# Performance work log

Hardware: AMD Instinct MI355X
Metric: run time of the kernel (lower is better)

Reference implementation:

```python
import jax, jax.numpy as jnp
import numpy as np

USER_NUM = 100000
ITEM_NUM = 100000  # padding index; table has ITEM_NUM+1 rows
D = 64
B = 4096
L = 200
NEG_WEIGHT = 0.1


def setup_inputs() -> dict:
    key = jax.random.key(0)
    k1, k2, k3, k4, k5 = jax.random.split(key, 5)
    uids = jax.random.randint(k1, (B,), 0, USER_NUM, dtype=jnp.int64 if jax.config.jax_enable_x64 else jnp.int32)
    pos_iids = jax.random.randint(k2, (B, L), 0, ITEM_NUM + 1, dtype=jnp.int64 if jax.config.jax_enable_x64 else jnp.int32)
    user_W = jax.random.normal(k3, (USER_NUM, D), dtype=jnp.float32) * 0.1
    item_W = jax.random.normal(k4, (ITEM_NUM + 1, D), dtype=jnp.float32) * 0.1
    h = jnp.full((D, 1), 0.01, dtype=jnp.float32)  # reset_para: constant 0.01
    return {"uids": uids, "pos_iids": pos_iids, "user_W": user_W, "item_W": item_W, "h": h}


def reference(uids, pos_iids, user_W, item_W, h):
    u_emb = user_W[uids]                      # [B, D] (dropout p=0 -> identity)
    pos_embs = item_W[pos_iids]               # [B, L, D]
    mask = (pos_iids != ITEM_NUM).astype(u_emb.dtype)  # padding id masked out
    pos_embs = pos_embs * mask[:, :, None]
    # hpq[b,l] = sum_d u[b,d] * pos[b,l,d] * h[d]
    hpq = jnp.einsum('bd,bld,d->bl', u_emb, pos_embs, h[:, 0])
    pos_data_loss = jnp.sum((1.0 - NEG_WEIGHT) * jnp.square(hpq) - 2.0 * hpq)
    # part_1/part_2 in torch are sums of per-row outer products == Gram matrices
    part_1 = item_W.T @ item_W                # [D, D]
    part_2 = u_emb.T @ u_emb                  # [D, D]
    part_3 = h @ h.T                          # [D, D]
    all_data_loss = jnp.sum(part_1 * part_2 * part_3)
    return NEG_WEIGHT * all_data_loss + pos_data_loss
```

## Files before the change

### kernel.cpp

```cpp
#include <hip/hip_runtime.h>

#define D 64
#define ITEM_PAD 100000
#define LSEQ 200
#define BATCH 4096
#define NEG_W 0.1f
#define NBI 512
#define NBU 64


__global__ void gram_kernel(const float* __restrict__ W, const int* __restrict__ idx,
                            int nrows, float* __restrict__ out, int partial) {
    __shared__ float tile[16 * D];
    const int t  = threadIdx.x;
    const int ti = t >> 4;
    const int tj = t & 15;

    float acc[4][4] = {{0.f,0.f,0.f,0.f},{0.f,0.f,0.f,0.f},
                       {0.f,0.f,0.f,0.f},{0.f,0.f,0.f,0.f}};

    const int nchunks = (nrows + 15) >> 4;
    for (int c = blockIdx.x; c < nchunks; c += gridDim.x) {
        const int r = (c << 4) + ti;
        float4 v = make_float4(0.f, 0.f, 0.f, 0.f);
        if (r < nrows) {
            const int src = idx ? idx[r] : r;
            v = *(const float4*)(W + (size_t)src * D + tj * 4);
        }
        __syncthreads();
        *(float4*)(tile + ti * D + tj * 4) = v;
        __syncthreads();

        #pragma unroll
        for (int r2 = 0; r2 < 16; ++r2) {
            float xi[4], xj[4];
            *(float4*)xi = *(const float4*)(tile + r2 * D + ti * 4);
            *(float4*)xj = *(const float4*)(tile + r2 * D + tj * 4);
            #pragma unroll
            for (int a = 0; a < 4; ++a)
                #pragma unroll
                for (int b2 = 0; b2 < 4; ++b2)
                    acc[a][b2] += xi[a] * xj[b2];
        }
    }

    if (partial) {
        float* dst = out + (size_t)blockIdx.x * 4096;
        #pragma unroll
        for (int a = 0; a < 4; ++a)
            *(float4*)(dst + (ti * 4 + a) * D + tj * 4) = *(const float4*)acc[a];
    } else {
        #pragma unroll
        for (int a = 0; a < 4; ++a)
            #pragma unroll
            for (int b2 = 0; b2 < 4; ++b2)
                atomicAdd(out + (ti * 4 + a) * D + (tj * 4 + b2), acc[a][b2]);
    }
}

__global__ void reduce_gram_kernel(float* __restrict__ ws) {
    const float* Pi = ws + 12288;
    const float* Pu = ws + 12288 + (size_t)NBI * 4096;
    const int b = blockIdx.x, t = threadIdx.x;
    if (b < 256) {
        const int k  = (b & 15) * 256 + t;
        const int p0 = (b >> 4) * (NBI / 16);
        float s = 0.f;
        #pragma unroll 4
        for (int p = 0; p < NBI / 16; ++p) s += Pi[(size_t)(p0 + p) * 4096 + k];
        atomicAdd(ws + k, s);
    } else {
        const int bb = b - 256;
        const int k  = (bb & 15) * 256 + t;
        const int p0 = (bb >> 4) * (NBU / 4);
        float s = 0.f;
        #pragma unroll 4
        for (int p = 0; p < NBU / 4; ++p) s += Pu[(size_t)(p0 + p) * 4096 + k];
        atomicAdd(ws + 4096 + k, s);
    }
}

__global__ void pos_loss_kernel(const int* __restrict__ uids,
                                const int* __restrict__ pos_iids,
                                const float* __restrict__ user_W,
                                const float* __restrict__ item_W,
                                const float* __restrict__ h,
                                float* __restrict__ out, int partial) {
    __shared__ float uh[D];
    __shared__ int sidx[LSEQ];
    __shared__ float red[4];
    const int b = blockIdx.x;
    const int t = threadIdx.x;

    if (t < LSEQ) sidx[t] = pos_iids[(size_t)b * LSEQ + t];
    if (t >= 192) {
        const int j = t - 192;
        uh[j] = user_W[(size_t)uids[b] * D + j] * h[j];
    }
    __syncthreads();

    const int lane = t & 63;
    const int wave = t >> 6;
    const int p    = lane >> 4;
    const int q    = lane & 15;
    const int base = wave * 4 + p;

    const float4 u4 = *(const float4*)(uh + q * 4);

    int ids[13];
    #pragma unroll
    for (int k = 0; k < 13; ++k) {
        const int l = base + 16 * k;
        ids[k] = (l < LSEQ) ? sidx[l] : ITEM_PAD;
    }

    float4 rows[13];
    #pragma unroll
    for (int k = 0; k < 13; ++k) {
        float4 v = make_float4(0.f, 0.f, 0.f, 0.f);
        if (ids[k] != ITEM_PAD)
            v = *(const float4*)(item_W + (size_t)ids[k] * D + q * 4);
        rows[k] = v;
    }

    float local = 0.f;
    #pragma unroll
    for (int k = 0; k < 13; ++k) {
        float s = u4.x * rows[k].x + u4.y * rows[k].y + u4.z * rows[k].z + u4.w * rows[k].w;
        s += __shfl_xor(s, 1);
        s += __shfl_xor(s, 2);
        s += __shfl_xor(s, 4);
        s += __shfl_xor(s, 8);
        if (q == 0)
            local += (1.0f - NEG_W) * s * s - 2.0f * s;
    }

    local += __shfl_xor(local, 1);
    local += __shfl_xor(local, 2);
    local += __shfl_xor(local, 4);
    local += __shfl_xor(local, 8);
    local += __shfl_xor(local, 16);
    local += __shfl_xor(local, 32);
    if (lane == 0) red[wave] = local;
    __syncthreads();
    if (t == 0) {
        const float tot = red[0] + red[1] + red[2] + red[3];
        if (partial) out[b] = tot;
        else atomicAdd(out, tot);
    }
}

__global__ void finalize_kernel(const float* __restrict__ ws,
                                const float* __restrict__ h,
                                float* __restrict__ out, int npos) {
    __shared__ float red[4];
    const int t = threadIdx.x;
    float s = 0.f;
    for (int k = t; k < 4096; k += 256) {
        const int i = k >> 6, j = k & 63;
        s += ws[k] * ws[4096 + k] * h[i] * h[j];
    }
    float ps = 0.f;
    for (int k = t; k < npos; k += 256) ps += ws[8192 + k];
    float v = NEG_W * s + ps;
    v += __shfl_xor(v, 1);
    v += __shfl_xor(v, 2);
    v += __shfl_xor(v, 4);
    v += __shfl_xor(v, 8);
    v += __shfl_xor(v, 16);
    v += __shfl_xor(v, 32);
    const int lane = t & 63, wave = t >> 6;
    if (lane == 0) red[wave] = v;
    __syncthreads();
    if (t == 0) out[0] = red[0] + red[1] + red[2] + red[3];
}

extern "C" void kernel_launch(void* const* d_in, const int* in_sizes, int n_in,
                              void* d_out, int out_size, void* d_ws, size_t ws_size,
                              hipStream_t stream) {
    const int*   uids     = (const int*)d_in[0];
    const int*   pos_iids = (const int*)d_in[1];
    const float* user_W   = (const float*)d_in[2];
    const float* item_W   = (const float*)d_in[3];
    const float* h        = (const float*)d_in[4];
    float* out = (float*)d_out;
    float* ws  = (float*)d_ws;

    const size_t need = (size_t)(12288 + (NBI + NBU) * 4096) * sizeof(float);
    if (ws_size >= need) {
        hipMemsetAsync(ws, 0, 8192 * sizeof(float), stream);
        gram_kernel<<<NBI, 256, 0, stream>>>(item_W, nullptr, ITEM_PAD + 1,
                                             ws + 12288, 1);
        gram_kernel<<<NBU, 256, 0, stream>>>(user_W, uids, BATCH,
                                             ws + 12288 + (size_t)NBI * 4096, 1);
        pos_loss_kernel<<<BATCH, 256, 0, stream>>>(uids, pos_iids, user_W, item_W, h,
                                                   ws + 8192, 1);
        reduce_gram_kernel<<<320, 256, 0, stream>>>(ws);
        finalize_kernel<<<1, 256, 0, stream>>>(ws, h, out, 4096);
    } else {
        hipMemsetAsync(ws, 0, (8192 + 1) * sizeof(float), stream);
        gram_kernel<<<256, 256, 0, stream>>>(item_W, nullptr, ITEM_PAD + 1, ws, 0);
        gram_kernel<<<64, 256, 0, stream>>>(user_W, uids, BATCH, ws + 4096, 0);
        pos_loss_kernel<<<BATCH, 256, 0, stream>>>(uids, pos_iids, user_W, item_W, h,
                                                   ws + 8192, 0);
        finalize_kernel<<<1, 256, 0, stream>>>(ws, h, out, 1);
    }
}
```

Baseline: 150.9 us.

## Fuse gram and positive-loss kernels into one launch, drop memset and atomics

```diff
diff --git a/kernel.cpp b/kernel.cpp
--- a/kernel.cpp
+++ b/kernel.cpp
@@ -7,170 +7,178 @@
 #define NEG_W 0.1f
 #define NBI 512
 #define NBU 64
-
-
-__global__ void gram_kernel(const float* __restrict__ W, const int* __restrict__ idx,
-                            int nrows, float* __restrict__ out, int partial) {
-    __shared__ float tile[16 * D];
+#define GSZ (D * D)
+#define PITEM_OFF 0
+#define PUSER_OFF ((size_t)NBI * GSZ)
+#define POS_OFF   (PUSER_OFF + (size_t)NBU * GSZ)
+#define WS2_OFF   (POS_OFF + BATCH)
+#define WS_FLOATS (WS2_OFF + 256)
+
+__global__ void fused_partials(const int* __restrict__ uids,
+                               const int* __restrict__ pos_iids,
+                               const float* __restrict__ user_W,
+                               const float* __restrict__ item_W,
+                               const float* __restrict__ h,
+                               float* __restrict__ ws) {
+    __shared__ float smem[16 * D];
+    const int bid = blockIdx.x;
+    const int t   = threadIdx.x;
+
+    if (bid < NBI + NBU) {
+        const bool item = (bid < NBI);
+        const float* __restrict__ W = item ? item_W : user_W;
+        const int* __restrict__ idx = item ? nullptr : uids;
+        const int nrows   = item ? (ITEM_PAD + 1) : BATCH;
+        const int stride  = item ? NBI : NBU;
+        const int b0      = item ? bid : bid - NBI;
+        float* __restrict__ out =
+            ws + (item ? PITEM_OFF + (size_t)b0 * GSZ : PUSER_OFF + (size_t)b0 * GSZ);
+
+        const int ti = t >> 4;
+        const int tj = t & 15;
+        float acc[4][4] = {{0.f,0.f,0.f,0.f},{0.f,0.f,0.f,0.f},
+                           {0.f,0.f,0.f,0.f},{0.f,0.f,0.f,0.f}};
+
+        const int nchunks = (nrows + 15) >> 4;
+        for (int c = b0; c < nchunks; c += stride) {
+            const int r = (c << 4) + ti;
+            float4 v = make_float4(0.f, 0.f, 0.f, 0.f);
+            if (r < nrows) {
+                const int src = idx ? idx[r] : r;
+                v = *(const float4*)(W + (size_t)src * D + tj * 4);
+            }
+            __syncthreads();
+            *(float4*)(smem + ti * D + tj * 4) = v;
+            __syncthreads();
+
+            #pragma unroll
+            for (int r2 = 0; r2 < 16; ++r2) {
+                float xi[4], xj[4];
+                *(float4*)xi = *(const float4*)(smem + r2 * D + ti * 4);
+                *(float4*)xj = *(const float4*)(smem + r2 * D + tj * 4);
+                #pragma unroll
+                for (int a = 0; a < 4; ++a)
+                    #pragma unroll
+                    for (int b2 = 0; b2 < 4; ++b2)
+                        acc[a][b2] += xi[a] * xj[b2];
+            }
+        }
+        #pragma unroll
+        for (int a = 0; a < 4; ++a)
+            *(float4*)(out + (ti * 4 + a) * D + tj * 4) = *(const float4*)acc[a];
+    } else {
+        const int b = bid - (NBI + NBU);
+        float* uh  = smem;
+        int*   sidx = (int*)(smem + D);
+        float* red = smem + D + LSEQ;
+
+        if (t < LSEQ) sidx[t] = pos_iids[(size_t)b * LSEQ + t];
+        if (t >= 192) {
+            const int j = t - 192;
+            uh[j] = user_W[(size_t)uids[b] * D + j] * h[j];
+        }
+        __syncthreads();
+
+        const int lane = t & 63;
+        const int wave = t >> 6;
+        const int p    = lane >> 4;
+        const int q    = lane & 15;
+        const int base = wave * 4 + p;
+
+        const float4 u4 = *(const float4*)(uh + q * 4);
+
+        int ids[13];
+        #pragma unroll
+        for (int k = 0; k < 13; ++k) {
+            const int l = base + 16 * k;
+            ids[k] = (l < LSEQ) ? sidx[l] : ITEM_PAD;
+        }
+        float4 rows[13];
+        #pragma unroll
+        for (int k = 0; k < 13; ++k) {
+            float4 v = make_float4(0.f, 0.f, 0.f, 0.f);
+            if (ids[k] != ITEM_PAD)
+                v = *(const float4*)(item_W + (size_t)ids[k] * D + q * 4);
+            rows[k] = v;
+        }
+
+        float local = 0.f;
+        #pragma unroll
+        for (int k = 0; k < 13; ++k) {
+            float s = u4.x*rows[k].x + u4.y*rows[k].y + u4.z*rows[k].z + u4.w*rows[k].w;
+            s += __shfl_xor(s, 1);
+            s += __shfl_xor(s, 2);
+            s += __shfl_xor(s, 4);
+            s += __shfl_xor(s, 8);
+            if (q == 0)
+                local += (1.0f - NEG_W) * s * s - 2.0f * s;
+        }
+        local += __shfl_xor(local, 1);
+        local += __shfl_xor(local, 2);
+        local += __shfl_xor(local, 4);
+        local += __shfl_xor(local, 8);
+        local += __shfl_xor(local, 16);
+        local += __shfl_xor(local, 32);
+        if (lane == 0) red[wave] = local;
+        __syncthreads();
+        if (t == 0)
+            ws[POS_OFF + b] = red[0] + red[1] + red[2] + red[3];
+    }
+}
+
+__global__ void reduce_partials(const float* __restrict__ ws,
+                                const float* __restrict__ h,
+                                float* __restrict__ ws2) {
+    __shared__ float rI[4][16];
+    __shared__ float rU[4][16];
+    const int b  = blockIdx.x;
     const int t  = threadIdx.x;
-    const int ti = t >> 4;
-    const int tj = t & 15;
-
-    float acc[4][4] = {{0.f,0.f,0.f,0.f},{0.f,0.f,0.f,0.f},
-                       {0.f,0.f,0.f,0.f},{0.f,0.f,0.f,0.f}};
-
-    const int nchunks = (nrows + 15) >> 4;
-    for (int c = blockIdx.x; c < nchunks; c += gridDim.x) {
-        const int r = (c << 4) + ti;
-        float4 v = make_float4(0.f, 0.f, 0.f, 0.f);
-        if (r < nrows) {
-            const int src = idx ? idx[r] : r;
-            v = *(const float4*)(W + (size_t)src * D + tj * 4);
-        }
-        __syncthreads();
-        *(float4*)(tile + ti * D + tj * 4) = v;
-        __syncthreads();
-
-        #pragma unroll
-        for (int r2 = 0; r2 < 16; ++r2) {
-            float xi[4], xj[4];
-            *(float4*)xi = *(const float4*)(tile + r2 * D + ti * 4);
-            *(float4*)xj = *(const float4*)(tile + r2 * D + tj * 4);
-            #pragma unroll
-            for (int a = 0; a < 4; ++a)
-                #pragma unroll
-                for (int b2 = 0; b2 < 4; ++b2)
-                    acc[a][b2] += xi[a] * xj[b2];
-        }
-    }
-
-    if (partial) {
-        float* dst = out + (size_t)blockIdx.x * 4096;
-        #pragma unroll
-        for (int a = 0; a < 4; ++a)
-            *(float4*)(dst + (ti * 4 + a) * D + tj * 4) = *(const float4*)acc[a];
-    } else {
-        #pragma unroll
-        for (int a = 0; a < 4; ++a)
-            #pragma unroll
-            for (int b2 = 0; b2 < 4; ++b2)
-                atomicAdd(out + (ti * 4 + a) * D + (tj * 4 + b2), acc[a][b2]);
-    }
-}
-
-__global__ void reduce_gram_kernel(float* __restrict__ ws) {
-    const float* Pi = ws + 12288;
-    const float* Pu = ws + 12288 + (size_t)NBI * 4096;
-    const int b = blockIdx.x, t = threadIdx.x;
-    if (b < 256) {
-        const int k  = (b & 15) * 256 + t;
-        const int p0 = (b >> 4) * (NBI / 16);
-        float s = 0.f;
-        #pragma unroll 4
-        for (int p = 0; p < NBI / 16; ++p) s += Pi[(size_t)(p0 + p) * 4096 + k];
-        atomicAdd(ws + k, s);
-    } else {
-        const int bb = b - 256;
-        const int k  = (bb & 15) * 256 + t;
-        const int p0 = (bb >> 4) * (NBU / 4);
-        float s = 0.f;
-        #pragma unroll 4
-        for (int p = 0; p < NBU / 4; ++p) s += Pu[(size_t)(p0 + p) * 4096 + k];
-        atomicAdd(ws + 4096 + k, s);
-    }
-}
-
-__global__ void pos_loss_kernel(const int* __restrict__ uids,
-                                const int* __restrict__ pos_iids,
-                                const float* __restrict__ user_W,
-                                const float* __restrict__ item_W,
-                                const float* __restrict__ h,
-                                float* __restrict__ out, int partial) {
-    __shared__ float uh[D];
-    __shared__ int sidx[LSEQ];
-    __shared__ float red[4];
-    const int b = blockIdx.x;
-    const int t = threadIdx.x;
-
-    if (t < LSEQ) sidx[t] = pos_iids[(size_t)b * LSEQ + t];
-    if (t >= 192) {
-        const int j = t - 192;
-        uh[j] = user_W[(size_t)uids[b] * D + j] * h[j];
-    }
-    __syncthreads();
-
+    const int kk = t & 15;
+    const int ps = t >> 4;
     const int lane = t & 63;
     const int wave = t >> 6;
-    const int p    = lane >> 4;
-    const int q    = lane & 15;
-    const int base = wave * 4 + p;
-
-    const float4 u4 = *(const float4*)(uh + q * 4);
-
-    int ids[13];
+    const int k  = b * 16 + kk;
+
+    float si = 0.f, su = 0.f;
+    #pragma unroll 8
+    for (int p = ps; p < NBI; p += 16) si += ws[PITEM_OFF + (size_t)p * GSZ + k];
     #pragma unroll
-    for (int k = 0; k < 13; ++k) {
-        const int l = base + 16 * k;
-        ids[k] = (l < LSEQ) ? sidx[l] : ITEM_PAD;
+    for (int p = ps; p < NBU; p += 16) su += ws[PUSER_OFF + (size_t)p * GSZ + k];
+
+    si += __shfl_xor(si, 16); si += __shfl_xor(si, 32);
+    su += __shfl_xor(su, 16); su += __shfl_xor(su, 32);
+    if (lane < 16) { rI[wave][kk] = si; rU[wave][kk] = su; }
+    __syncthreads();
+
+    float c = 0.f;
+    if (t < 16) {
+        const float Gi = rI[0][t] + rI[1][t] + rI[2][t] + rI[3][t];
+        const float Gu = rU[0][t] + rU[1][t] + rU[2][t] + rU[3][t];
+        const int kg = b * 16 + t;
+        const int i = kg >> 6, j = kg & 63;
+        c = NEG_W * Gi * Gu * h[i] * h[j] + ws[POS_OFF + b * 16 + t];
     }
-
-    float4 rows[13];
-    #pragma unroll
-    for (int k = 0; k < 13; ++k) {
-        float4 v = make_float4(0.f, 0.f, 0.f, 0.f);
-        if (ids[k] != ITEM_PAD)
-            v = *(const float4*)(item_W + (size_t)ids[k] * D + q * 4);
-        rows[k] = v;
+    if (wave == 0) {
+        c += __shfl_xor(c, 1);
+        c += __shfl_xor(c, 2);
+        c += __shfl_xor(c, 4);
+        c += __shfl_xor(c, 8);
+        if (lane == 0) ws2[b] = c;
     }
-
-    float local = 0.f;
-    #pragma unroll
-    for (int k = 0; k < 13; ++k) {
-        float s = u4.x * rows[k].x + u4.y * rows[k].y + u4.z * rows[k].z + u4.w * rows[k].w;
-        s += __shfl_xor(s, 1);
-        s += __shfl_xor(s, 2);
-        s += __shfl_xor(s, 4);
-        s += __shfl_xor(s, 8);
-        if (q == 0)
-            local += (1.0f - NEG_W) * s * s - 2.0f * s;
-    }
-
-    local += __shfl_xor(local, 1);
-    local += __shfl_xor(local, 2);
-    local += __shfl_xor(local, 4);
-    local += __shfl_xor(local, 8);
-    local += __shfl_xor(local, 16);
-    local += __shfl_xor(local, 32);
-    if (lane == 0) red[wave] = local;
-    __syncthreads();
-    if (t == 0) {
-        const float tot = red[0] + red[1] + red[2] + red[3];
-        if (partial) out[b] = tot;
-        else atomicAdd(out, tot);
-    }
-}
-
-__global__ void finalize_kernel(const float* __restrict__ ws,
-                                const float* __restrict__ h,
-                                float* __restrict__ out, int npos) {
+}
+
+__global__ void final_sum(const float* __restrict__ ws2, float* __restrict__ out) {
     __shared__ float red[4];
     const int t = threadIdx.x;
-    float s = 0.f;
-    for (int k = t; k < 4096; k += 256) {
-        const int i = k >> 6, j = k & 63;
-        s += ws[k] * ws[4096 + k] * h[i] * h[j];
-    }
-    float ps = 0.f;
-    for (int k = t; k < npos; k += 256) ps += ws[8192 + k];
-    float v = NEG_W * s + ps;
-    v += __shfl_xor(v, 1);
-    v += __shfl_xor(v, 2);
-    v += __shfl_xor(v, 4);
-    v += __shfl_xor(v, 8);
-    v += __shfl_xor(v, 16);
-    v += __shfl_xor(v, 32);
+    float s = ws2[t];
+    s += __shfl_xor(s, 1);
+    s += __shfl_xor(s, 2);
+    s += __shfl_xor(s, 4);
+    s += __shfl_xor(s, 8);
+    s += __shfl_xor(s, 16);
+    s += __shfl_xor(s, 32);
     const int lane = t & 63, wave = t >> 6;
-    if (lane == 0) red[wave] = v;
+    if (lane == 0) red[wave] = s;
     __syncthreads();
     if (t == 0) out[0] = red[0] + red[1] + red[2] + red[3];
 }
@@ -186,23 +194,8 @@
     float* out = (float*)d_out;
     float* ws  = (float*)d_ws;
 
-    const size_t need = (size_t)(12288 + (NBI + NBU) * 4096) * sizeof(float);
-    if (ws_size >= need) {
-        hipMemsetAsync(ws, 0, 8192 * sizeof(float), stream);
-        gram_kernel<<<NBI, 256, 0, stream>>>(item_W, nullptr, ITEM_PAD + 1,
-                                             ws + 12288, 1);
-        gram_kernel<<<NBU, 256, 0, stream>>>(user_W, uids, BATCH,
-                                             ws + 12288 + (size_t)NBI * 4096, 1);
-        pos_loss_kernel<<<BATCH, 256, 0, stream>>>(uids, pos_iids, user_W, item_W, h,
-                                                   ws + 8192, 1);
-        reduce_gram_kernel<<<320, 256, 0, stream>>>(ws);
-        finalize_kernel<<<1, 256, 0, stream>>>(ws, h, out, 4096);
-    } else {
-        hipMemsetAsync(ws, 0, (8192 + 1) * sizeof(float), stream);
-        gram_kernel<<<256, 256, 0, stream>>>(item_W, nullptr, ITEM_PAD + 1, ws, 0);
-        gram_kernel<<<64, 256, 0, stream>>>(user_W, uids, BATCH, ws + 4096, 0);
-        pos_loss_kernel<<<BATCH, 256, 0, stream>>>(uids, pos_iids, user_W, item_W, h,
-                                                   ws + 8192, 0);
-        finalize_kernel<<<1, 256, 0, stream>>>(ws, h, out, 1);
-    }
-}
+    fused_partials<<<NBI + NBU + BATCH, 256, 0, stream>>>(uids, pos_iids, user_W,
+                                                          item_W, h, ws);
+    reduce_partials<<<256, 256, 0, stream>>>(ws, h, ws + WS2_OFF);
+    final_sum<<<1, 256, 0, stream>>>(ws + WS2_OFF, out);
+}
```

Result: faster. 126.3 us (-16.3%).
